# Optimization experiments

Hardware: AMD Instinct MI355X
Metric: run time of the kernel (lower is better)

The kernel has to match this reference:

```python
import jax, jax.numpy as jnp
import numpy as np

# Model dims (from init_kwargs + mamba_ssm defaults)
D_MODEL = 1024
N_LAYER = 2
D_STATE = 16
D_CONV = 4
D_INNER = 2 * D_MODEL          # expand=2
DT_RANK = D_MODEL // 16        # 64
VOCAB = 32000
BATCH, SEQLEN = 2, 1024


def setup_inputs() -> dict:
    key = jax.random.key(0)
    ks = jax.random.split(key, 10)
    s = 0.02
    x = jax.random.randint(ks[0], (BATCH, SEQLEN), 0, VOCAB)
    embedding = jax.random.normal(ks[1], (VOCAB, D_MODEL), dtype=jnp.float32) * s
    norm_w = jnp.ones((N_LAYER, D_MODEL), dtype=jnp.float32)
    in_proj_w = jax.random.normal(ks[2], (N_LAYER, 2 * D_INNER, D_MODEL), dtype=jnp.float32) * s
    conv_w = jax.random.normal(ks[3], (N_LAYER, D_INNER, D_CONV), dtype=jnp.float32) * (1.0 / np.sqrt(D_CONV))
    conv_b = jnp.zeros((N_LAYER, D_INNER), dtype=jnp.float32)
    x_proj_w = jax.random.normal(ks[4], (N_LAYER, DT_RANK + 2 * D_STATE, D_INNER), dtype=jnp.float32) * s
    dt_proj_w = jax.random.normal(ks[5], (N_LAYER, D_INNER, DT_RANK), dtype=jnp.float32) * (DT_RANK ** -0.5)
    # inverse-softplus of dt_init ~ 0.01 (mamba default dt range)
    dt_bias = jnp.full((N_LAYER, D_INNER), float(np.log(np.expm1(0.01))), dtype=jnp.float32)
    A_log = jnp.log(jnp.broadcast_to(jnp.arange(1, D_STATE + 1, dtype=jnp.float32), (N_LAYER, D_INNER, D_STATE)))
    D = jnp.ones((N_LAYER, D_INNER), dtype=jnp.float32)
    out_proj_w = jax.random.normal(ks[6], (N_LAYER, D_MODEL, D_INNER), dtype=jnp.float32) * s
    final_norm_w = jnp.ones((D_MODEL,), dtype=jnp.float32)
    return {"x": x, "embedding": embedding, "norm_w": norm_w, "in_proj_w": in_proj_w,
            "conv_w": conv_w, "conv_b": conv_b, "x_proj_w": x_proj_w, "dt_proj_w": dt_proj_w,
            "dt_bias": dt_bias, "A_log": A_log, "D": D, "out_proj_w": out_proj_w,
            "final_norm_w": final_norm_w}


def _rmsnorm(h, w, eps=1e-5):
    return h * jax.lax.rsqrt(jnp.mean(h * h, axis=-1, keepdims=True) + eps) * w


def _scan_combine(c1, c2):
    a1, b1 = c1
    a2, b2 = c2
    return a2 * a1, a2 * b1 + b2


def _mamba_block(h, norm_w, in_proj_w, conv_w, conv_b, x_proj_w, dt_proj_w, dt_bias, A_log, D, out_proj_w):
    u = _rmsnorm(h, norm_w)
    xz = jnp.einsum('bld,ed->ble', u, in_proj_w)           # [B,L,2*D_INNER]
    xi, z = jnp.split(xz, 2, axis=-1)
    # depthwise causal conv1d, kernel D_CONV
    k = conv_w.T[:, None, :]                               # [D_CONV, 1, D_INNER]
    xc = jax.lax.conv_general_dilated(xi, k, (1,), [(D_CONV - 1, 0)],
                                      dimension_numbers=('NLC', 'LIO', 'NLC'),
                                      feature_group_count=D_INNER) + conv_b
    xc = jax.nn.silu(xc)
    dbl = jnp.einsum('bld,ed->ble', xc, x_proj_w)          # [B,L,DT_RANK+2*D_STATE]
    dt_low = dbl[..., :DT_RANK]
    Bm = dbl[..., DT_RANK:DT_RANK + D_STATE]
    Cm = dbl[..., DT_RANK + D_STATE:]
    dt = jax.nn.softplus(jnp.einsum('blr,dr->bld', dt_low, dt_proj_w) + dt_bias)
    A = -jnp.exp(A_log)                                    # [D_INNER, D_STATE]
    a = jnp.exp(dt[..., None] * A)                         # [B,L,D_INNER,D_STATE]
    b = dt[..., None] * Bm[:, :, None, :] * xc[..., None]  # [B,L,D_INNER,D_STATE]
    hs = jax.lax.associative_scan(_scan_combine, (a, b), axis=1)[1]
    y = jnp.einsum('bldn,bln->bld', hs, Cm) + xc * D
    y = y * jax.nn.silu(z)
    return h + jnp.einsum('bld,md->blm', y, out_proj_w)


def reference(x, embedding, norm_w, in_proj_w, conv_w, conv_b, x_proj_w, dt_proj_w,
              dt_bias, A_log, D, out_proj_w, final_norm_w):
    h = embedding[x]                                       # [B,L,D_MODEL]
    for i in range(N_LAYER):
        h = _mamba_block(h, norm_w[i], in_proj_w[i], conv_w[i], conv_b[i], x_proj_w[i],
                         dt_proj_w[i], dt_bias[i], A_log[i], D[i], out_proj_w[i])
    h = _rmsnorm(h, final_norm_w)
    logits = jnp.einsum('bld,vd->blv', h, embedding)       # tied lm head
    return logits
```

## Files before the change

kernel.cpp:

```cpp
#include <hip/hip_runtime.h>
#include <hip/hip_bf16.h>
#include <math.h>

#define D_MODEL 1024
#define N_LAYER 2
#define D_STATE 16
#define D_CONV  4
#define D_INNER 2048
#define DT_RANK 64
#define VOCAB   32000
#define BATCH   2
#define SEQLEN  1024
#define TOKENS  (BATCH*SEQLEN)
#define NC      32
#define CL      32

typedef __hip_bfloat16 bf16;
typedef __bf16 bf16x8 __attribute__((ext_vector_type(8)));
typedef float f32x4 __attribute__((ext_vector_type(4)));

__device__ inline void gld_lds16(const bf16* g, bf16* l) {
    __builtin_amdgcn_global_load_lds(
        (const __attribute__((address_space(1))) void*)g,
        (__attribute__((address_space(3))) void*)l, 16, 0, 0);
}

__device__ inline float softplus_fast(float v) {
    return (v > 20.f) ? v : __logf(1.f + __expf(v));
}
__device__ inline float silu_fast(float v) {
    return v / (1.f + __expf(-v));
}

__global__ __launch_bounds__(256) void embed_kernel(const int* __restrict__ x,
                                                    const float* __restrict__ emb,
                                                    float* __restrict__ h) {
    int t = blockIdx.x;
    int tok = x[t];
    const float4* src = (const float4*)(emb + (size_t)tok * D_MODEL);
    float4* dst = (float4*)(h + (size_t)t * D_MODEL);
    dst[threadIdx.x] = src[threadIdx.x];
}

__global__ __launch_bounds__(256) void rmsnorm_bf16(const float* __restrict__ h,
                                                    const float* __restrict__ w,
                                                    bf16* __restrict__ u) {
    int t = blockIdx.x;
    const float4* hv = (const float4*)(h + (size_t)t * D_MODEL);
    float4 v = hv[threadIdx.x];
    float ss = v.x*v.x + v.y*v.y + v.z*v.z + v.w*v.w;
    #pragma unroll
    for (int off = 32; off > 0; off >>= 1) ss += __shfl_down(ss, off);
    __shared__ float red[4];
    int lane = threadIdx.x & 63, wid = threadIdx.x >> 6;
    if (lane == 0) red[wid] = ss;
    __syncthreads();
    float tot = red[0] + red[1] + red[2] + red[3];
    float scale = rsqrtf(tot * (1.0f / (float)D_MODEL) + 1e-5f);
    float4 wq = ((const float4*)w)[threadIdx.x];
    size_t o = (size_t)t * D_MODEL + threadIdx.x * 4;
    u[o+0] = __float2bfloat16(v.x * scale * wq.x);
    u[o+1] = __float2bfloat16(v.y * scale * wq.y);
    u[o+2] = __float2bfloat16(v.z * scale * wq.z);
    u[o+3] = __float2bfloat16(v.w * scale * wq.w);
}

__global__ __launch_bounds__(256) void f32_to_bf16(const float* __restrict__ s,
                                                   bf16* __restrict__ d, int n) {
    int i = (blockIdx.x * 256 + threadIdx.x) * 4;
    if (i < n) {
        float4 v = *(const float4*)(s + i);
        d[i+0] = __float2bfloat16(v.x);
        d[i+1] = __float2bfloat16(v.y);
        d[i+2] = __float2bfloat16(v.z);
        d[i+3] = __float2bfloat16(v.w);
    }
}

__global__ __launch_bounds__(256) void conv_xproj_pad(const float* __restrict__ s,
                                                      bf16* __restrict__ d) {
    int col = blockIdx.x * 256 + threadIdx.x;
    int row = blockIdx.y;
    int layer = blockIdx.z;
    float v = (row < 96) ? s[((size_t)layer * 96 + row) * D_INNER + col] : 0.f;
    d[((size_t)layer * 128 + row) * D_INNER + col] = __float2bfloat16(v);
}

__global__ __launch_bounds__(256) void gemm_bf16(
    const bf16* __restrict__ A, int lda,
    const bf16* __restrict__ W, int ldw,
    float* __restrict__ C, int ldc,
    int N, int K, int acc, int swz, int M)
{
    __shared__ bf16 lds[2][2][128 * 64];
    int bx = blockIdx.x, by = blockIdx.y;
    if (swz) {
        int bid = by * gridDim.x + bx;
        int q = (gridDim.x * gridDim.y) >> 3;
        int n = (bid & 7) * q + (bid >> 3);
        by = n % gridDim.y;
        bx = n / gridDim.y;
    }
    const int z = blockIdx.z;
    A += (size_t)z * K;
    W += (size_t)z * K;
    C += (size_t)z * M * (size_t)ldc;

    const int tid  = threadIdx.x;
    const int wave = tid >> 6;
    const int lane = tid & 63;
    const int wr = wave >> 1, wc = wave & 1;
    const size_t rowBase = (size_t)by * 128;
    const size_t colBase = (size_t)bx * 128;

    const int srow = 8 * wave + (lane >> 3);
    const int scol = ((lane & 7) ^ (lane >> 3)) << 3;
    const bf16* aGs = A + (rowBase + srow) * (size_t)lda + scol;
    const bf16* bGs = W + (colBase + srow) * (size_t)ldw + scol;

#define STAGE(tt, bb) do {                                                      \
        const size_t kofs_ = (size_t)(tt) * 64;                                 \
        _Pragma("unroll")                                                       \
        for (int i_ = 0; i_ < 4; ++i_) {                                        \
            gld_lds16(aGs + kofs_ + (size_t)(32 * i_) * lda,                    \
                      &lds[bb][0][(32 * i_ + 8 * wave) * 64]);                  \
            gld_lds16(bGs + kofs_ + (size_t)(32 * i_) * ldw,                    \
                      &lds[bb][1][(32 * i_ + 8 * wave) * 64]);                  \
        }                                                                       \
    } while (0)

    f32x4 accv[4][4];
    #pragma unroll
    for (int i = 0; i < 4; ++i)
        #pragma unroll
        for (int j = 0; j < 4; ++j)
            accv[i][j] = f32x4{0.f, 0.f, 0.f, 0.f};

    const int arow0 = wr * 64 + (lane & 15);
    const int brow0 = wc * 64 + (lane & 15);
    const int h8  = (lane >> 4) << 3;
    const int sw8 = (lane & 7) << 3;

    const int NT = K >> 6;
    STAGE(0, 0);
    for (int t = 0; t < NT; ++t) {
        const int cur = t & 1;
        if (t + 1 < NT) {
            STAGE(t + 1, cur ^ 1);
            asm volatile("s_waitcnt vmcnt(8)" ::: "memory");
        } else {
            asm volatile("s_waitcnt vmcnt(0)" ::: "memory");
        }
        __builtin_amdgcn_s_barrier();

        const bf16* Ab = &lds[cur][0][0];
        const bf16* Bb = &lds[cur][1][0];
        #pragma unroll
        for (int kk = 0; kk < 2; ++kk) {
            const int cs = ((kk << 5) + h8) ^ sw8;
            bf16x8 af[4], bv[4];
            #pragma unroll
            for (int i = 0; i < 4; ++i)
                af[i] = *(const bf16x8*)(Ab + (arow0 + 16 * i) * 64 + cs);
            #pragma unroll
            for (int j = 0; j < 4; ++j)
                bv[j] = *(const bf16x8*)(Bb + (brow0 + 16 * j) * 64 + cs);
            #pragma unroll
            for (int i = 0; i < 4; ++i)
                #pragma unroll
                for (int j = 0; j < 4; ++j)
                    accv[i][j] = __builtin_amdgcn_mfma_f32_16x16x32_bf16(
                        af[i], bv[j], accv[i][j], 0, 0, 0);
        }
        asm volatile("s_waitcnt lgkmcnt(0)" ::: "memory");
        __builtin_amdgcn_s_barrier();
    }
#undef STAGE

    const int cl = lane & 15;
    const int rg = (lane >> 4) * 4;
    #pragma unroll
    for (int i = 0; i < 4; ++i) {
        #pragma unroll
        for (int j = 0; j < 4; ++j) {
            int col = (int)colBase + wc * 64 + j * 16 + cl;
            if (col < N) {
                size_t base = (rowBase + wr * 64 + i * 16 + rg) * (size_t)ldc + col;
                #pragma unroll
                for (int r = 0; r < 4; ++r) {
                    size_t idx = base + (size_t)r * ldc;
                    C[idx] = acc ? C[idx] + accv[i][j][r] : accv[i][j][r];
                }
            }
        }
    }
}

__global__ __launch_bounds__(256) void conv_silu_kernel(const float* __restrict__ xz,
                                                        const float* __restrict__ cw,
                                                        const float* __restrict__ cb,
                                                        float* __restrict__ xcf,
                                                        bf16* __restrict__ xcb) {
    int d = blockIdx.x * 256 + threadIdx.x;
    int l0 = blockIdx.y * 8;
    int b = blockIdx.z;
    float w0 = cw[d*4+0], w1 = cw[d*4+1], w2 = cw[d*4+2], w3 = cw[d*4+3];
    float bias = cb[d];
    float win0 = (l0 >= 3) ? xz[((size_t)b * SEQLEN + l0 - 3) * (2*D_INNER) + d] : 0.f;
    float win1 = (l0 >= 2) ? xz[((size_t)b * SEQLEN + l0 - 2) * (2*D_INNER) + d] : 0.f;
    float win2 = (l0 >= 1) ? xz[((size_t)b * SEQLEN + l0 - 1) * (2*D_INNER) + d] : 0.f;
    #pragma unroll
    for (int i = 0; i < 8; ++i) {
        float cur = xz[((size_t)b * SEQLEN + l0 + i) * (2*D_INNER) + d];
        float acc = bias + w0*win0 + w1*win1 + w2*win2 + w3*cur;
        float s = silu_fast(acc);
        size_t o = ((size_t)b * SEQLEN + l0 + i) * D_INNER + d;
        xcf[o] = s;
        xcb[o] = __float2bfloat16(s);
        win0 = win1; win1 = win2; win2 = cur;
    }
}

__global__ __launch_bounds__(256) void reduce_xproj(const float* __restrict__ px,
                                                    float* __restrict__ dblf,
                                                    bf16* __restrict__ dbl_b) {
    int i = blockIdx.x * 256 + threadIdx.x;
    float s = 0.f;
    #pragma unroll
    for (int z = 0; z < 8; ++z) s += px[(size_t)z * (TOKENS*96) + i];
    dblf[i] = s;
    dbl_b[i] = __float2bfloat16(s);
}

__global__ __launch_bounds__(256) void reduce_oproj(const float* __restrict__ po,
                                                    float* __restrict__ h) {
    int i = (blockIdx.x * 256 + threadIdx.x) * 4;
    float4 a = *(const float4*)(po + i);
    float4 b = *(const float4*)(po + (size_t)TOKENS*D_MODEL + i);
    float4 hv = *(const float4*)(h + i);
    hv.x += a.x + b.x; hv.y += a.y + b.y; hv.z += a.z + b.z; hv.w += a.w + b.w;
    *(float4*)(h + i) = hv;
}

__global__ __launch_bounds__(256) void scan_chunk(const float* __restrict__ dtp,
                                                  const float* __restrict__ dt_bias,
                                                  const float* __restrict__ dbl,
                                                  const float* __restrict__ xc,
                                                  const float* __restrict__ A_log,
                                                  float* __restrict__ aprod,
                                                  float* __restrict__ sfin) {
    int d = blockIdx.x * 256 + threadIdx.x;
    int c = blockIdx.y;
    int b = blockIdx.z;
    __shared__ float Bs[CL][D_STATE];
    for (int i = threadIdx.x; i < CL * D_STATE; i += 256) {
        int l = i >> 4, n = i & 15;
        Bs[l][n] = dbl[((size_t)b * SEQLEN + c * CL + l) * 96 + DT_RANK + n];
    }
    __syncthreads();
    float A[D_STATE];
    #pragma unroll
    for (int n = 0; n < D_STATE; ++n) A[n] = -__expf(A_log[d * D_STATE + n]);
    float bias = dt_bias[d];
    float st[D_STATE];
    #pragma unroll
    for (int n = 0; n < D_STATE; ++n) st[n] = 0.f;
    float dts = 0.f;
    for (int l = 0; l < CL; ++l) {
        size_t t = (size_t)b * SEQLEN + c * CL + l;
        float dtv = softplus_fast(dtp[t * D_INNER + d] + bias);
        dts += dtv;
        float dx = dtv * xc[t * D_INNER + d];
        #pragma unroll
        for (int n = 0; n < D_STATE; ++n) {
            float a = __expf(dtv * A[n]);
            st[n] = a * st[n] + dx * Bs[l][n];
        }
    }
    #pragma unroll
    for (int n = 0; n < D_STATE; ++n) {
        size_t o = (((size_t)b * NC + c) * D_STATE + n) * D_INNER + d;
        aprod[o] = __expf(dts * A[n]);
        sfin[o] = st[n];
    }
}

__global__ __launch_bounds__(256) void scan_carry(const float* __restrict__ aprod,
                                                  const float* __restrict__ sfin,
                                                  float* __restrict__ initS) {
    int idx = blockIdx.x * 256 + threadIdx.x;
    int d = idx & (D_INNER - 1);
    int n = (idx >> 11) & (D_STATE - 1);
    int b = idx >> 15;
    float st = 0.f;
    for (int c = 0; c < NC; ++c) {
        size_t o = (((size_t)b * NC + c) * D_STATE + n) * D_INNER + d;
        initS[o] = st;
        st = aprod[o] * st + sfin[o];
    }
}

__global__ __launch_bounds__(256) void scan_emit(const float* __restrict__ dtp,
                                                 const float* __restrict__ dt_bias,
                                                 const float* __restrict__ dbl,
                                                 const float* __restrict__ xc,
                                                 const float* __restrict__ xz,
                                                 const float* __restrict__ A_log,
                                                 const float* __restrict__ Dp,
                                                 const float* __restrict__ initS,
                                                 bf16* __restrict__ y) {
    int d = blockIdx.x * 256 + threadIdx.x;
    int c = blockIdx.y;
    int b = blockIdx.z;
    __shared__ float BCs[CL][2 * D_STATE];
    for (int i = threadIdx.x; i < CL * 2 * D_STATE; i += 256) {
        int l = i >> 5, n = i & 31;
        BCs[l][n] = dbl[((size_t)b * SEQLEN + c * CL + l) * 96 + DT_RANK + n];
    }
    __syncthreads();
    float A[D_STATE];
    #pragma unroll
    for (int n = 0; n < D_STATE; ++n) A[n] = -__expf(A_log[d * D_STATE + n]);
    float bias = dt_bias[d];
    float Dv = Dp[d];
    float st[D_STATE];
    #pragma unroll
    for (int n = 0; n < D_STATE; ++n)
        st[n] = initS[(((size_t)b * NC + c) * D_STATE + n) * D_INNER + d];
    for (int l = 0; l < CL; ++l) {
        size_t t = (size_t)b * SEQLEN + c * CL + l;
        float dtv = softplus_fast(dtp[t * D_INNER + d] + bias);
        float xcv = xc[t * D_INNER + d];
        float dx = dtv * xcv;
        float acc = 0.f;
        #pragma unroll
        for (int n = 0; n < D_STATE; ++n) {
            float a = __expf(dtv * A[n]);
            st[n] = a * st[n] + dx * BCs[l][n];
            acc += st[n] * BCs[l][D_STATE + n];
        }
        acc += xcv * Dv;
        float zv = xz[t * (2 * D_INNER) + D_INNER + d];
        y[t * D_INNER + d] = __float2bfloat16(acc * silu_fast(zv));
    }
}

extern "C" void kernel_launch(void* const* d_in, const int* in_sizes, int n_in,
                              void* d_out, int out_size, void* d_ws, size_t ws_size,
                              hipStream_t stream) {
    const int*   x          = (const int*)  d_in[0];
    const float* emb        = (const float*)d_in[1];
    const float* norm_w     = (const float*)d_in[2];
    const float* in_proj_w  = (const float*)d_in[3];
    const float* conv_w     = (const float*)d_in[4];
    const float* conv_b     = (const float*)d_in[5];
    const float* x_proj_w   = (const float*)d_in[6];
    const float* dt_proj_w  = (const float*)d_in[7];
    const float* dt_bias    = (const float*)d_in[8];
    const float* A_log      = (const float*)d_in[9];
    const float* Dp         = (const float*)d_in[10];
    const float* out_proj_w = (const float*)d_in[11];
    const float* fnorm_w    = (const float*)d_in[12];
    float* out = (float*)d_out;
    float* ws  = (float*)d_ws;

    bf16*  embf   = (bf16*)ws;
    bf16*  u_b    = (bf16*)(ws + 16384000);
    float* xz     = ws + 17432576;
    float* xc_f   = ws + 25821184;
    bf16*  xc_b   = (bf16*)(ws + 30015488);
    float* dtp    = ws + 32112640;
    float* h      = ws + 36306944;
    float* dblf   = ws + 38404096;
    bf16*  dbl_b  = (bf16*)(ws + 38600704);
    bf16*  y_b    = (bf16*)(ws + 38699008);
    bf16*  inpj_b = (bf16*)(ws + 40796160);
    bf16*  xpj_b  = (bf16*)(ws + 44990464);
    bf16*  dtpj_b = (bf16*)(ws + 45252608);
    bf16*  otpj_b = (bf16*)(ws + 45383680);
    float* aprod  = ws + 47480832;
    float* sfin   = ws + 49577984;
    float* initS  = ws + 51675136;
    float* px     = ws + 53772288;
    float* po     = ws + 55345152;

    f32_to_bf16<<<(VOCAB*D_MODEL/4 + 255)/256, 256, 0, stream>>>(emb, embf, VOCAB*D_MODEL);
    f32_to_bf16<<<(2*2*D_INNER*D_MODEL/4 + 255)/256, 256, 0, stream>>>(in_proj_w,  inpj_b, 2*2*D_INNER*D_MODEL);
    conv_xproj_pad<<<dim3(D_INNER/256, 128, N_LAYER), 256, 0, stream>>>(x_proj_w, xpj_b);
    f32_to_bf16<<<(2*D_INNER*DT_RANK/4 + 255)/256, 256, 0, stream>>>(dt_proj_w,  dtpj_b, 2*D_INNER*DT_RANK);
    f32_to_bf16<<<(2*D_MODEL*D_INNER/4 + 255)/256, 256, 0, stream>>>(out_proj_w, otpj_b, 2*D_MODEL*D_INNER);

    embed_kernel<<<TOKENS, 256, 0, stream>>>(x, emb, h);

    for (int layer = 0; layer < N_LAYER; ++layer) {
        rmsnorm_bf16<<<TOKENS, 256, 0, stream>>>(h, norm_w + layer * D_MODEL, u_b);
        gemm_bf16<<<dim3(4096/128, TOKENS/128), 256, 0, stream>>>(
            u_b, D_MODEL, inpj_b + (size_t)layer * 2 * D_INNER * D_MODEL, D_MODEL,
            xz, 2 * D_INNER, 2 * D_INNER, D_MODEL, 0, 1, TOKENS);
        conv_silu_kernel<<<dim3(D_INNER/256, SEQLEN/8, BATCH), 256, 0, stream>>>(
            xz, conv_w + (size_t)layer * D_INNER * D_CONV, conv_b + layer * D_INNER,
            xc_f, xc_b);
        gemm_bf16<<<dim3(1, TOKENS/128, 8), 256, 0, stream>>>(
            xc_b, D_INNER, xpj_b + (size_t)layer * 128 * D_INNER, D_INNER,
            px, 96, 96, 256, 0, 0, TOKENS);
        reduce_xproj<<<(TOKENS*96)/256, 256, 0, stream>>>(px, dblf, dbl_b);
        gemm_bf16<<<dim3(D_INNER/128, TOKENS/128), 256, 0, stream>>>(
            dbl_b, 96, dtpj_b + (size_t)layer * D_INNER * DT_RANK, DT_RANK,
            dtp, D_INNER, D_INNER, DT_RANK, 0, 1, TOKENS);
        scan_chunk<<<dim3(D_INNER/256, NC, BATCH), 256, 0, stream>>>(
            dtp, dt_bias + layer * D_INNER, dblf, xc_f,
            A_log + (size_t)layer * D_INNER * D_STATE, aprod, sfin);
        scan_carry<<<(BATCH*D_STATE*D_INNER)/256, 256, 0, stream>>>(aprod, sfin, initS);
        scan_emit<<<dim3(D_INNER/256, NC, BATCH), 256, 0, stream>>>(
            dtp, dt_bias + layer * D_INNER, dblf, xc_f, xz,
            A_log + (size_t)layer * D_INNER * D_STATE, Dp + layer * D_INNER,
            initS, y_b);
        gemm_bf16<<<dim3(D_MODEL/128, TOKENS/128, 2), 256, 0, stream>>>(
            y_b, D_INNER, otpj_b + (size_t)layer * D_MODEL * D_INNER, D_INNER,
            po, D_MODEL, D_MODEL, 1024, 0, 1, TOKENS);
        reduce_oproj<<<(TOKENS*D_MODEL/4)/256, 256, 0, stream>>>(po, h);
    }

    rmsnorm_bf16<<<TOKENS, 256, 0, stream>>>(h, fnorm_w, u_b);

    gemm_bf16<<<dim3(VOCAB/128, TOKENS/128), 256, 0, stream>>>(
        u_b, D_MODEL, embf, D_MODEL,
        out, VOCAB, VOCAB, D_MODEL, 0, 1, TOKENS);
}
```

Baseline: 547.4 us.

## Fuse embedding bf16 conversion into vocab GEMM and store xz as bf16

Drops the separate fp32-to-bf16 pass over the 32000x1024 embedding table. A dedicated vocab GEMM now loads the fp32 embedding rows into registers, converts them and writes bf16 into LDS, double-buffered, and writes logits with nontemporal stores. The in_proj GEMM now writes xz as bf16, halving that buffer's traffic for the conv and scan kernels at a small precision cost. The register-staged B path may expose more load latency than the direct global-to-LDS loads it replaces.

```diff
diff --git a/kernel.cpp b/kernel.cpp
--- a/kernel.cpp
+++ b/kernel.cpp
@@ -30,6 +30,13 @@
 }
 __device__ inline float silu_fast(float v) {
     return v / (1.f + __expf(-v));
+}
+
+__device__ inline bf16x8 cvt8(float4 a, float4 b) {
+    bf16x8 r;
+    r[0] = (__bf16)a.x; r[1] = (__bf16)a.y; r[2] = (__bf16)a.z; r[3] = (__bf16)a.w;
+    r[4] = (__bf16)b.x; r[5] = (__bf16)b.y; r[6] = (__bf16)b.z; r[7] = (__bf16)b.w;
+    return r;
 }
 
 __global__ __launch_bounds__(256) void embed_kernel(const int* __restrict__ x,
@@ -90,7 +97,7 @@
     const bf16* __restrict__ A, int lda,
     const bf16* __restrict__ W, int ldw,
     float* __restrict__ C, int ldc,
-    int N, int K, int acc, int swz, int M)
+    int N, int K, int acc, int swz, int M, int bfout)
 {
     __shared__ bf16 lds[2][2][128 * 64];
     int bx = blockIdx.x, by = blockIdx.y;
@@ -186,17 +193,137 @@
             int col = (int)colBase + wc * 64 + j * 16 + cl;
             if (col < N) {
                 size_t base = (rowBase + wr * 64 + i * 16 + rg) * (size_t)ldc + col;
-                #pragma unroll
-                for (int r = 0; r < 4; ++r) {
-                    size_t idx = base + (size_t)r * ldc;
-                    C[idx] = acc ? C[idx] + accv[i][j][r] : accv[i][j][r];
+                if (bfout) {
+                    bf16* Cb = (bf16*)C;
+                    #pragma unroll
+                    for (int r = 0; r < 4; ++r)
+                        Cb[base + (size_t)r * ldc] = __float2bfloat16(accv[i][j][r]);
+                } else {
+                    #pragma unroll
+                    for (int r = 0; r < 4; ++r) {
+                        size_t idx = base + (size_t)r * ldc;
+                        C[idx] = acc ? C[idx] + accv[i][j][r] : accv[i][j][r];
+                    }
                 }
             }
         }
     }
 }
 
-__global__ __launch_bounds__(256) void conv_silu_kernel(const float* __restrict__ xz,
+__global__ __launch_bounds__(256) void gemm_vocab(
+    const bf16* __restrict__ A,
+    const float* __restrict__ W,
+    float* __restrict__ C)
+{
+    __shared__ bf16 ldsA[2][128 * 64];
+    __shared__ bf16 ldsB[2][128 * 64];
+    int bx = blockIdx.x, by = blockIdx.y;
+    {
+        int bid = by * gridDim.x + bx;
+        int q = (gridDim.x * gridDim.y) >> 3;
+        int n = (bid & 7) * q + (bid >> 3);
+        by = n % gridDim.y;
+        bx = n / gridDim.y;
+    }
+    const int tid  = threadIdx.x;
+    const int wave = tid >> 6;
+    const int lane = tid & 63;
+    const int wr = wave >> 1, wc = wave & 1;
+    const size_t rowBase = (size_t)by * 128;
+    const size_t colBase = (size_t)bx * 128;
+
+    const int srow = 8 * wave + (lane >> 3);
+    const int scol = ((lane & 7) ^ (lane >> 3)) << 3;
+    const int bcs  = (lane & 7) << 3;
+    const bf16*  aGs = A + (rowBase + srow) * (size_t)D_MODEL + scol;
+    const float* bGs = W + (colBase + srow) * (size_t)D_MODEL + bcs;
+
+    f32x4 accv[4][4];
+    #pragma unroll
+    for (int i = 0; i < 4; ++i)
+        #pragma unroll
+        for (int j = 0; j < 4; ++j)
+            accv[i][j] = f32x4{0.f, 0.f, 0.f, 0.f};
+
+    const int arow0 = wr * 64 + (lane & 15);
+    const int brow0 = wc * 64 + (lane & 15);
+    const int h8  = (lane >> 4) << 3;
+    const int sw8 = (lane & 7) << 3;
+
+    const int NT = D_MODEL / 64;
+    float4 br0[4], br1[4];
+
+    #pragma unroll
+    for (int i = 0; i < 4; ++i) {
+        gld_lds16(aGs + (size_t)(32 * i) * D_MODEL, &ldsA[0][(32 * i + 8 * wave) * 64]);
+        br0[i] = *(const float4*)(bGs + (size_t)(32 * i) * D_MODEL);
+        br1[i] = *(const float4*)(bGs + (size_t)(32 * i) * D_MODEL + 4);
+    }
+    asm volatile("s_waitcnt vmcnt(0)" ::: "memory");
+    #pragma unroll
+    for (int i = 0; i < 4; ++i)
+        *(bf16x8*)(&ldsB[0][(32 * i + srow) * 64 + scol]) = cvt8(br0[i], br1[i]);
+
+    for (int t = 0; t < NT; ++t) {
+        const int cur = t & 1;
+        asm volatile("s_waitcnt lgkmcnt(0)" ::: "memory");
+        __builtin_amdgcn_s_barrier();
+
+        if (t + 1 < NT) {
+            const size_t ko = (size_t)(t + 1) * 64;
+            #pragma unroll
+            for (int i = 0; i < 4; ++i) {
+                gld_lds16(aGs + ko + (size_t)(32 * i) * D_MODEL,
+                          &ldsA[cur ^ 1][(32 * i + 8 * wave) * 64]);
+                br0[i] = *(const float4*)(bGs + ko + (size_t)(32 * i) * D_MODEL);
+                br1[i] = *(const float4*)(bGs + ko + (size_t)(32 * i) * D_MODEL + 4);
+            }
+        }
+
+        const bf16* Ab = &ldsA[cur][0];
+        const bf16* Bb = &ldsB[cur][0];
+        #pragma unroll
+        for (int kk = 0; kk < 2; ++kk) {
+            const int cs = ((kk << 5) + h8) ^ sw8;
+            bf16x8 af[4], bv[4];
+            #pragma unroll
+            for (int i = 0; i < 4; ++i)
+                af[i] = *(const bf16x8*)(Ab + (arow0 + 16 * i) * 64 + cs);
+            #pragma unroll
+            for (int j = 0; j < 4; ++j)
+                bv[j] = *(const bf16x8*)(Bb + (brow0 + 16 * j) * 64 + cs);
+            #pragma unroll
+            for (int i = 0; i < 4; ++i)
+                #pragma unroll
+                for (int j = 0; j < 4; ++j)
+                    accv[i][j] = __builtin_amdgcn_mfma_f32_16x16x32_bf16(
+                        af[i], bv[j], accv[i][j], 0, 0, 0);
+        }
+
+        if (t + 1 < NT) {
+            asm volatile("s_waitcnt vmcnt(0)" ::: "memory");
+            #pragma unroll
+            for (int i = 0; i < 4; ++i)
+                *(bf16x8*)(&ldsB[cur ^ 1][(32 * i + srow) * 64 + scol]) = cvt8(br0[i], br1[i]);
+        }
+    }
+
+    const int cl = lane & 15;
+    const int rg = (lane >> 4) * 4;
+    #pragma unroll
+    for (int i = 0; i < 4; ++i) {
+        #pragma unroll
+        for (int j = 0; j < 4; ++j) {
+            int col = (int)colBase + wc * 64 + j * 16 + cl;
+            size_t base = (rowBase + wr * 64 + i * 16 + rg) * (size_t)VOCAB + col;
+            #pragma unroll
+            for (int r = 0; r < 4; ++r)
+                __builtin_nontemporal_store(accv[i][j][r], &C[base + (size_t)r * VOCAB]);
+        }
+    }
+}
+
+__global__ __launch_bounds__(256) void conv_silu_kernel(const bf16* __restrict__ xz,
                                                         const float* __restrict__ cw,
                                                         const float* __restrict__ cb,
                                                         float* __restrict__ xcf,
@@ -206,12 +333,12 @@
     int b = blockIdx.z;
     float w0 = cw[d*4+0], w1 = cw[d*4+1], w2 = cw[d*4+2], w3 = cw[d*4+3];
     float bias = cb[d];
-    float win0 = (l0 >= 3) ? xz[((size_t)b * SEQLEN + l0 - 3) * (2*D_INNER) + d] : 0.f;
-    float win1 = (l0 >= 2) ? xz[((size_t)b * SEQLEN + l0 - 2) * (2*D_INNER) + d] : 0.f;
-    float win2 = (l0 >= 1) ? xz[((size_t)b * SEQLEN + l0 - 1) * (2*D_INNER) + d] : 0.f;
+    float win0 = (l0 >= 3) ? __bfloat162float(xz[((size_t)b * SEQLEN + l0 - 3) * (2*D_INNER) + d]) : 0.f;
+    float win1 = (l0 >= 2) ? __bfloat162float(xz[((size_t)b * SEQLEN + l0 - 2) * (2*D_INNER) + d]) : 0.f;
+    float win2 = (l0 >= 1) ? __bfloat162float(xz[((size_t)b * SEQLEN + l0 - 1) * (2*D_INNER) + d]) : 0.f;
     #pragma unroll
     for (int i = 0; i < 8; ++i) {
-        float cur = xz[((size_t)b * SEQLEN + l0 + i) * (2*D_INNER) + d];
+        float cur = __bfloat162float(xz[((size_t)b * SEQLEN + l0 + i) * (2*D_INNER) + d]);
         float acc = bias + w0*win0 + w1*win1 + w2*win2 + w3*cur;
         float s = silu_fast(acc);
         size_t o = ((size_t)b * SEQLEN + l0 + i) * D_INNER + d;
@@ -304,7 +431,7 @@
                                                  const float* __restrict__ dt_bias,
                                                  const float* __restrict__ dbl,
                                                  const float* __restrict__ xc,
-                                                 const float* __restrict__ xz,
+                                                 const bf16* __restrict__ xz,
                                                  const float* __restrict__ A_log,
                                                  const float* __restrict__ Dp,
                                                  const float* __restrict__ initS,
@@ -340,7 +467,7 @@
             acc += st[n] * BCs[l][D_STATE + n];
         }
         acc += xcv * Dv;
-        float zv = xz[t * (2 * D_INNER) + D_INNER + d];
+        float zv = __bfloat162float(xz[t * (2 * D_INNER) + D_INNER + d]);
         y[t * D_INNER + d] = __float2bfloat16(acc * silu_fast(zv));
     }
 }
@@ -364,9 +491,8 @@
     float* out = (float*)d_out;
     float* ws  = (float*)d_ws;
 
-    bf16*  embf   = (bf16*)ws;
     bf16*  u_b    = (bf16*)(ws + 16384000);
-    float* xz     = ws + 17432576;
+    bf16*  xz_b   = (bf16*)(ws + 17432576);
     float* xc_f   = ws + 25821184;
     bf16*  xc_b   = (bf16*)(ws + 30015488);
     float* dtp    = ws + 32112640;
@@ -384,7 +510,6 @@
     float* px     = ws + 53772288;
     float* po     = ws + 55345152;
 
-    f32_to_bf16<<<(VOCAB*D_MODEL/4 + 255)/256, 256, 0, stream>>>(emb, embf, VOCAB*D_MODEL);
     f32_to_bf16<<<(2*2*D_INNER*D_MODEL/4 + 255)/256, 256, 0, stream>>>(in_proj_w,  inpj_b, 2*2*D_INNER*D_MODEL);
     conv_xproj_pad<<<dim3(D_INNER/256, 128, N_LAYER), 256, 0, stream>>>(x_proj_w, xpj_b);
     f32_to_bf16<<<(2*D_INNER*DT_RANK/4 + 255)/256, 256, 0, stream>>>(dt_proj_w,  dtpj_b, 2*D_INNER*DT_RANK);
@@ -396,34 +521,32 @@
         rmsnorm_bf16<<<TOKENS, 256, 0, stream>>>(h, norm_w + layer * D_MODEL, u_b);
         gemm_bf16<<<dim3(4096/128, TOKENS/128), 256, 0, stream>>>(
             u_b, D_MODEL, inpj_b + (size_t)layer * 2 * D_INNER * D_MODEL, D_MODEL,
-            xz, 2 * D_INNER, 2 * D_INNER, D_MODEL, 0, 1, TOKENS);
+            (float*)xz_b, 2 * D_INNER, 2 * D_INNER, D_MODEL, 0, 1, TOKENS, 1);
         conv_silu_kernel<<<dim3(D_INNER/256, SEQLEN/8, BATCH), 256, 0, stream>>>(
-            xz, conv_w + (size_t)layer * D_INNER * D_CONV, conv_b + layer * D_INNER,
+            xz_b, conv_w + (size_t)layer * D_INNER * D_CONV, conv_b + layer * D_INNER,
             xc_f, xc_b);
         gemm_bf16<<<dim3(1, TOKENS/128, 8), 256, 0, stream>>>(
             xc_b, D_INNER, xpj_b + (size_t)layer * 128 * D_INNER, D_INNER,
-            px, 96, 96, 256, 0, 0, TOKENS);
+            px, 96, 96, 256, 0, 0, TOKENS, 0);
         reduce_xproj<<<(TOKENS*96)/256, 256, 0, stream>>>(px, dblf, dbl_b);
         gemm_bf16<<<dim3(D_INNER/128, TOKENS/128), 256, 0, stream>>>(
             dbl_b, 96, dtpj_b + (size_t)layer * D_INNER * DT_RANK, DT_RANK,
-            dtp, D_INNER, D_INNER, DT_RANK, 0, 1, TOKENS);
+            dtp, D_INNER, D_INNER, DT_RANK, 0, 1, TOKENS, 0);
         scan_chunk<<<dim3(D_INNER/256, NC, BATCH), 256, 0, stream>>>(
             dtp, dt_bias + layer * D_INNER, dblf, xc_f,
             A_log + (size_t)layer * D_INNER * D_STATE, aprod, sfin);
         scan_carry<<<(BATCH*D_STATE*D_INNER)/256, 256, 0, stream>>>(aprod, sfin, initS);
         scan_emit<<<dim3(D_INNER/256, NC, BATCH), 256, 0, stream>>>(
-            dtp, dt_bias + layer * D_INNER, dblf, xc_f, xz,
+            dtp, dt_bias + layer * D_INNER, dblf, xc_f, xz_b,
             A_log + (size_t)layer * D_INNER * D_STATE, Dp + layer * D_INNER,
             initS, y_b);
         gemm_bf16<<<dim3(D_MODEL/128, TOKENS/128, 2), 256, 0, stream>>>(
             y_b, D_INNER, otpj_b + (size_t)layer * D_MODEL * D_INNER, D_INNER,
-            po, D_MODEL, D_MODEL, 1024, 0, 1, TOKENS);
+            po, D_MODEL, D_MODEL, 1024, 0, 1, TOKENS, 0);
         reduce_oproj<<<(TOKENS*D_MODEL/4)/256, 256, 0, stream>>>(po, h);
     }
 
     rmsnorm_bf16<<<TOKENS, 256, 0, stream>>>(h, fnorm_w, u_b);
 
-    gemm_bf16<<<dim3(VOCAB/128, TOKENS/128), 256, 0, stream>>>(
-        u_b, D_MODEL, embf, D_MODEL,
-        out, VOCAB, VOCAB, D_MODEL, 0, 1, TOKENS);
-}
+    gemm_vocab<<<dim3(VOCAB/128, TOKENS/128), 256, 0, stream>>>(u_b, emb, out);
+}
```

Measured after the change: 649.9 us. 18.7% more time.
